# Kernel tuning notes

Measured on AMD Instinct MI355X. Metric: run time of the kernel, lower is better.

Reference implementation:

```python
import jax, jax.numpy as jnp
import numpy as np

B, S, D = 2, 2048, 3584
H, KV, HD = 28, 4, 128
N_REP = H // KV          # 7
MAX_S = 2048
SCALE = HD ** -0.5
ROPE_BASE = 1_000_000.0  # Qwen2 rope theta


def _rope_tables(max_s, hd, base):
    inv = 1.0 / (base ** (np.arange(0, hd, 2, dtype=np.float32) / hd))  # [hd/2]
    ang = np.arange(max_s, dtype=np.float32)[:, None] * inv[None, :]    # [S, hd/2]
    return jnp.asarray(np.cos(ang)), jnp.asarray(np.sin(ang))


def apply_rotary(x, cos, sin):
    # x: [b, s, h, hd] with interleaved complex pairs (torch view_as_complex layout)
    xr = x[..., 0::2]
    xi = x[..., 1::2]
    cos = cos[None, :, None, :]
    sin = sin[None, :, None, :]
    yr = xr * cos - xi * sin
    yi = xr * sin + xi * cos
    return jnp.stack([yr, yi], axis=-1).reshape(x.shape)


def setup_inputs() -> dict:
    key = jax.random.key(0)
    ks = jax.random.split(key, 8)
    w = 0.02
    x = jax.random.normal(ks[0], (B, S, D), jnp.float32)
    wq_w = jax.random.normal(ks[1], (H * HD, D), jnp.float32) * w
    wq_b = jax.random.normal(ks[2], (H * HD,), jnp.float32) * w
    wk_w = jax.random.normal(ks[3], (KV * HD, D), jnp.float32) * w
    wk_b = jax.random.normal(ks[4], (KV * HD,), jnp.float32) * w
    wv_w = jax.random.normal(ks[5], (KV * HD, D), jnp.float32) * w
    wv_b = jax.random.normal(ks[6], (KV * HD,), jnp.float32) * w
    wo_w = jax.random.normal(ks[7], (D, H * HD), jnp.float32) * w
    k_cache = jnp.zeros((B, MAX_S, KV, HD), jnp.float32)
    v_cache = jnp.zeros((B, MAX_S, KV, HD), jnp.float32)
    freqs_cos, freqs_sin = _rope_tables(MAX_S, HD, ROPE_BASE)
    # causal additive mask [s, t]; large-negative instead of -inf for safe grads
    mask = jnp.triu(jnp.full((S, S), -1e9, jnp.float32), k=1)
    return {"x": x, "wq_w": wq_w, "wq_b": wq_b, "wk_w": wk_w, "wk_b": wk_b,
            "wv_w": wv_w, "wv_b": wv_b, "wo_w": wo_w,
            "k_cache": k_cache, "v_cache": v_cache,
            "freqs_cos": freqs_cos, "freqs_sin": freqs_sin,
            "mask": mask, "start_pos": 0}


def reference(x, wq_w, wq_b, wk_w, wk_b, wv_w, wv_b, wo_w,
              k_cache, v_cache, freqs_cos, freqs_sin, mask, start_pos):
    bsz, seqlen, _ = x.shape
    end_pos = start_pos + seqlen
    q = (x @ wq_w.T + wq_b).reshape(bsz, seqlen, H, HD)
    k = (x @ wk_w.T + wk_b).reshape(bsz, seqlen, KV, HD)
    v = (x @ wv_w.T + wv_b).reshape(bsz, seqlen, KV, HD)
    cos = jax.lax.dynamic_slice_in_dim(freqs_cos, start_pos, seqlen, 0)
    sin = jax.lax.dynamic_slice_in_dim(freqs_sin, start_pos, seqlen, 0)
    q = apply_rotary(q, cos, sin)
    k = apply_rotary(k, cos, sin)
    # KV-cache write
    k_cache = jax.lax.dynamic_update_slice(k_cache, k, (0, start_pos, 0, 0))
    v_cache = jax.lax.dynamic_update_slice(v_cache, v, (0, start_pos, 0, 0))
    keys = k_cache[:bsz, :end_pos]    # [b, t, kv, hd]
    values = v_cache[:bsz, :end_pos]
    # GQA: repeat_interleave kv heads to n_heads
    keys = jnp.repeat(keys, N_REP, axis=2)      # [b, t, h, hd]
    values = jnp.repeat(values, N_REP, axis=2)
    scores = jnp.einsum('bshd,bthd->bsht', q, keys) * SCALE
    scores = scores + mask[None, :, None, :]
    probs = jax.nn.softmax(scores.astype(jnp.float32), axis=-1).astype(x.dtype)
    out = jnp.einsum('bsht,bthd->bshd', probs, values)
    out = out.reshape(bsz, seqlen, H * HD)
    return out @ wo_w.T
```

## Files before the change

### kernel.cpp

```cpp
#include <hip/hip_runtime.h>
#include <hip/hip_bf16.h>

typedef __attribute__((ext_vector_type(4)))  float  f32x4;
typedef __attribute__((ext_vector_type(16))) float  f32x16;
typedef __attribute__((ext_vector_type(8)))  __bf16 bf16x8;
typedef __attribute__((ext_vector_type(4)))  __bf16 bf16x4;
typedef __attribute__((ext_vector_type(4)))  unsigned int u32x4;

constexpr int S_LEN = 2048, DMODEL = 3584, NH = 28, NKV = 4, HD = 128, NREP = 7;
constexpr float SCALE_LOG2 = 0.1275174331f;

__device__ __forceinline__ unsigned int pack2(float a, float b) {
  unsigned short ua = __builtin_bit_cast(unsigned short, (__bf16)a);
  unsigned short ub = __builtin_bit_cast(unsigned short, (__bf16)b);
  return (unsigned int)ua | ((unsigned int)ub << 16);
}

__global__ void cvt5_kernel(const float* __restrict__ s0, const float* __restrict__ s1,
                            const float* __restrict__ s2, const float* __restrict__ s3,
                            const float* __restrict__ s4,
                            __bf16* __restrict__ d0, __bf16* __restrict__ d1,
                            __bf16* __restrict__ d2, __bf16* __restrict__ d3,
                            __bf16* __restrict__ d4,
                            int n0, int n1, int n2, int n3, int* __restrict__ ctr, int total) {
  if (blockIdx.x == 0 && threadIdx.x == 0) *ctr = 0;
  for (int i = blockIdx.x * blockDim.x + threadIdx.x; i < total; i += gridDim.x * blockDim.x) {
    const float* s; __bf16* d; int j = i;
    if (j < n0) { s = s0; d = d0; }
    else { j -= n0;
      if (j < n1) { s = s1; d = d1; }
      else { j -= n1;
        if (j < n2) { s = s2; d = d2; }
        else { j -= n2;
          if (j < n3) { s = s3; d = d3; }
          else { j -= n3; s = s4; d = d4; }
        }
      }
    }
    float4 v = reinterpret_cast<const float4*>(s)[j];
    bf16x4 o;
    o[0] = (__bf16)v.x; o[1] = (__bf16)v.y; o[2] = (__bf16)v.z; o[3] = (__bf16)v.w;
    reinterpret_cast<bf16x4*>(d)[j] = o;
  }
}

#define GLDS16(gsrc, ldst)                                                              \
  __builtin_amdgcn_global_load_lds((const __attribute__((address_space(1))) void*)(gsrc),\
                                   (__attribute__((address_space(3))) void*)(ldst), 16, 0, 0)

template <int MODE>
__global__ __launch_bounds__(512, 2) void gemm256(
    const __bf16* __restrict__ A, const __bf16* __restrict__ Bw,
    const float* __restrict__ bias, void* __restrict__ Cout,
    int M, int N, int K,
    const float* __restrict__ fcos, const float* __restrict__ fsin,
    const int* __restrict__ sp_ptr, float scale)
{
  extern __shared__ char smem[];
  const int tid = threadIdx.x;
  const int lane = tid & 63, wid = tid >> 6;
  const int wm = wid >> 2, wn = wid & 3;
  const int l31 = lane & 31, hh = lane >> 5;
  const int l15 = lane & 15;

  const int chunk = gridDim.x >> 3;
  const int wg = (blockIdx.x & 7) * chunk + (blockIdx.x >> 3);
  const int nbx = N >> 8;
  const int by = wg / nbx, bx = wg % nbx;
  const int row0 = by * 256, col0 = bx * 256;

  const int srL   = 16 * (tid >> 6) + ((tid >> 2) & 15);
  const int cperm = ((tid & 3) * 8) ^ (((tid >> 5) & 1) * 16);
  const __bf16* pA0 = A + (size_t)(row0 + srL) * K + cperm;
  const __bf16* pA1 = pA0 + (size_t)128 * K;
  const __bf16* pB0 = Bw + (size_t)(col0 + srL) * K + cperm;
  const __bf16* pB1 = pB0 + (size_t)128 * K;
  char* ldsA = smem + tid * 16;
  char* ldsB = smem + 65536 + tid * 16;

  const int laneoff = (l31 >> 4) * 1024 + l15 * 64 + hh * 16;
  const int ksx = (l31 & 8) << 2;
  const int abase = wm * 8192 + laneoff;
  const int R0 = wn * 64, R1 = wn * 64 + 32;
  const int bo0 = (R0 >> 7) * 8192 + ((R0 >> 4) & 7) * 1024;
  const int bo1 = (R1 >> 7) * 8192 + ((R1 >> 4) & 7) * 1024;

  f32x16 acc[4][2] = {};
  const int nt = K >> 5;

#pragma unroll
  for (int pt = 0; pt < 3; pt++) {
    const size_t ko = (size_t)pt * 32;
    char* sA = ldsA + pt * 16384;
    char* sB = ldsB + pt * 16384;
    GLDS16(pA0 + ko, sA);
    GLDS16(pA1 + ko, sA + 8192);
    GLDS16(pB0 + ko, sB);
    GLDS16(pB1 + ko, sB + 8192);
  }
  asm volatile("s_waitcnt vmcnt(8)" ::: "memory");
  __builtin_amdgcn_s_barrier();
  __builtin_amdgcn_sched_barrier(0);

  for (int t = 0; t < nt; t++) {
    const int slot = (t & 3) * 16384;
    const char* sa = smem + slot + abase;
    const char* sb = smem + slot + 65536 + laneoff;
    bf16x8 a0[4], a1[4], b0[2], b1[2];

    b0[0] = *reinterpret_cast<const bf16x8*>(sb + bo0 + ksx);
    b0[1] = *reinterpret_cast<const bf16x8*>(sb + bo1 + ksx);
#pragma unroll
    for (int fm = 0; fm < 4; fm++)
      a0[fm] = *reinterpret_cast<const bf16x8*>(sa + fm * 2048 + ksx);
    __builtin_amdgcn_sched_barrier(0);
    b1[0] = *reinterpret_cast<const bf16x8*>(sb + bo0 + (32 ^ ksx));
    b1[1] = *reinterpret_cast<const bf16x8*>(sb + bo1 + (32 ^ ksx));
#pragma unroll
    for (int fm = 0; fm < 4; fm++)
      a1[fm] = *reinterpret_cast<const bf16x8*>(sa + fm * 2048 + (32 ^ ksx));

    if (t + 3 < nt) {
      const size_t ko = (size_t)(t + 3) * 32;
      char* sA = ldsA + ((t + 3) & 3) * 16384;
      char* sB = ldsB + ((t + 3) & 3) * 16384;
      GLDS16(pA0 + ko, sA);
      GLDS16(pA1 + ko, sA + 8192);
      GLDS16(pB0 + ko, sB);
      GLDS16(pB1 + ko, sB + 8192);
    }

    asm volatile("s_waitcnt lgkmcnt(6)" ::: "memory");
    __builtin_amdgcn_sched_barrier(0);
    __builtin_amdgcn_s_setprio(1);
#pragma unroll
    for (int fn = 0; fn < 2; fn++)
#pragma unroll
      for (int fm = 0; fm < 4; fm++)
        acc[fm][fn] = __builtin_amdgcn_mfma_f32_32x32x16_bf16(a0[fm], b0[fn], acc[fm][fn], 0, 0, 0);
    __builtin_amdgcn_s_setprio(0);

    asm volatile("s_waitcnt lgkmcnt(0)" ::: "memory");
    __builtin_amdgcn_sched_barrier(0);
    __builtin_amdgcn_s_setprio(1);
#pragma unroll
    for (int fn = 0; fn < 2; fn++)
#pragma unroll
      for (int fm = 0; fm < 4; fm++)
        acc[fm][fn] = __builtin_amdgcn_mfma_f32_32x32x16_bf16(a1[fm], b1[fn], acc[fm][fn], 0, 0, 0);
    __builtin_amdgcn_s_setprio(0);

    if (t < nt - 3)       asm volatile("s_waitcnt vmcnt(8)" ::: "memory");
    else if (t == nt - 3) asm volatile("s_waitcnt vmcnt(4)" ::: "memory");
    else if (t == nt - 2) asm volatile("s_waitcnt vmcnt(0)" ::: "memory");
    __builtin_amdgcn_s_barrier();
    __builtin_amdgcn_sched_barrier(0);
  }

  if constexpr (MODE == 0) {
    float* C = (float*)Cout;
#pragma unroll
    for (int fm = 0; fm < 4; fm++) {
#pragma unroll
      for (int fn = 0; fn < 2; fn++) {
        const int col = col0 + wn * 64 + fn * 32 + l31;
#pragma unroll
        for (int r = 0; r < 16; r++) {
          const int row = row0 + wm * 128 + fm * 32 + (r & 3) + 8 * (r >> 2) + 4 * hh;
          C[(size_t)row * N + col] = acc[fm][fn][r];
        }
      }
    }
  } else {
    __bf16* C = (__bf16*)Cout;
    const int sp = sp_ptr[0];
    float bval[2];
#pragma unroll
    for (int fn = 0; fn < 2; fn++) bval[fn] = bias[col0 + wn * 64 + fn * 32 + l31];
#pragma unroll
    for (int fm = 0; fm < 4; fm++) {
#pragma unroll
      for (int fn = 0; fn < 2; fn++) {
        const int col = col0 + wn * 64 + fn * 32 + l31;
        const int i = (col & (HD - 1)) >> 1;
#pragma unroll
        for (int r = 0; r < 16; r++) {
          const int row = row0 + wm * 128 + fm * 32 + (r & 3) + 8 * (r >> 2) + 4 * hh;
          float y = acc[fm][fn][r] + bval[fn];
          float p = __shfl_xor(y, 1);
          const int spos = sp + (row & (S_LEN - 1));
          const float c = fcos[spos * (HD / 2) + i];
          const float sn = fsin[spos * (HD / 2) + i];
          y = (col & 1) ? (p * sn + y * c) : (y * c - p * sn);
          C[(size_t)row * N + col] = (__bf16)(y * scale);
        }
      }
    }
  }
}

__global__ __launch_bounds__(256) void gemm_kv(
    const __bf16* __restrict__ A,
    const __bf16* __restrict__ Wk, const float* __restrict__ bk, __bf16* __restrict__ Ko,
    const __bf16* __restrict__ Wv, const float* __restrict__ bv, __bf16* __restrict__ Vt,
    const float* __restrict__ fcos, const float* __restrict__ fsin,
    const int* __restrict__ sp_ptr)
{
  constexpr int N = 512, K = 3584;
  __shared__ __bf16 As[128 * 32];
  __shared__ __bf16 Bs[128 * 32];
  const int tid = threadIdx.x;
  const int lane = tid & 63, wid = tid >> 6;
  const int l15 = lane & 15, g = lane >> 4;
  const int wr = wid >> 1, wc = wid & 1;
  const bool isK = blockIdx.x < 4;
  const __bf16* Bw = isK ? Wk : Wv;
  const float* bias = isK ? bk : bv;
  const int row0 = blockIdx.y * 128;
  const int col0 = (blockIdx.x & 3) * 128;

  f32x4 acc[4][4] = {};

  const int srow = tid >> 2;
  const int scol = (tid & 3) * 8;
  const __bf16* Ag0 = A + (size_t)(row0 + srow) * K + scol;
  const __bf16* Ag1 = Ag0 + (size_t)64 * K;
  const __bf16* Bg0 = Bw + (size_t)(col0 + srow) * K + scol;
  const __bf16* Bg1 = Bg0 + (size_t)64 * K;
  __bf16* As0 = As + tid * 8;
  __bf16* As1 = As + 2048 + tid * 8;
  __bf16* Bs0 = Bs + tid * 8;
  __bf16* Bs1 = Bs + 2048 + tid * 8;

  for (int k0 = 0; k0 < K; k0 += 32) {
    GLDS16(Ag0 + k0, As0);
    GLDS16(Ag1 + k0, As1);
    GLDS16(Bg0 + k0, Bs0);
    GLDS16(Bg1 + k0, Bs1);
    __syncthreads();
    bf16x8 af[4], bfr[4];
#pragma unroll
    for (int m = 0; m < 4; m++)
      af[m] = *reinterpret_cast<const bf16x8*>(As + (wr * 64 + m * 16 + l15) * 32 + g * 8);
#pragma unroll
    for (int n = 0; n < 4; n++)
      bfr[n] = *reinterpret_cast<const bf16x8*>(Bs + (wc * 64 + n * 16 + l15) * 32 + g * 8);
#pragma unroll
    for (int m = 0; m < 4; m++)
#pragma unroll
      for (int n = 0; n < 4; n++)
        acc[m][n] = __builtin_amdgcn_mfma_f32_16x16x32_bf16(af[m], bfr[n], acc[m][n], 0, 0, 0);
    __syncthreads();
  }

  const int sp = sp_ptr[0];
  if (isK) {
#pragma unroll
    for (int m = 0; m < 4; m++) {
#pragma unroll
      for (int n = 0; n < 4; n++) {
        const int col = col0 + wc * 64 + n * 16 + l15;
        const float bval = bias[col];
        f32x4 v = acc[m][n];
#pragma unroll
        for (int r = 0; r < 4; r++) {
          const int row = row0 + wr * 64 + m * 16 + 4 * g + r;
          float y = v[r] + bval;
          float p = __shfl_xor(y, 1);
          const int i = (col & (HD - 1)) >> 1;
          const int spos = sp + (row & (S_LEN - 1));
          const float c = fcos[spos * (HD / 2) + i];
          const float sn = fsin[spos * (HD / 2) + i];
          y = (col & 1) ? (p * sn + y * c) : (y * c - p * sn);
          Ko[(size_t)row * N + col] = (__bf16)y;
        }
      }
    }
  } else {
    const int b4kv = ((row0 >> 11) * 4) + (blockIdx.x & 3);
    __bf16* vbase = Vt + ((size_t)b4kv << 18);
#pragma unroll
    for (int m = 0; m < 4; m++) {
#pragma unroll
      for (int n = 0; n < 4; n++) {
        const int d = wc * 64 + n * 16 + l15;
        const float bval = bias[col0 + d];
        const int s0 = (row0 + wr * 64 + m * 16 + 4 * g) & (S_LEN - 1);
        f32x4 v = acc[m][n];
        bf16x4 o;
#pragma unroll
        for (int r = 0; r < 4; r++) o[r] = (__bf16)(v[r] + bval);
        *reinterpret_cast<bf16x4*>(vbase + (size_t)d * S_LEN + s0) = o;
      }
    }
  }
}

__global__ __launch_bounds__(256, 2) void attn_kernel(
    const __bf16* __restrict__ Qb, const __bf16* __restrict__ Kb,
    const __bf16* __restrict__ Vt, __bf16* __restrict__ Ob, int* __restrict__ ctr)
{
  __shared__ __align__(16) char asmem[65536];
  __shared__ int jsh;

  const int tid = threadIdx.x, lane = tid & 63, wid = tid >> 6;
  const int l31 = lane & 31, hh = lane >> 5;

  const int trow = tid >> 4;
  const int kcol = (((tid & 15) * 16) ^ ((trow & 7) << 4)) >> 1;
  const int vrow = tid >> 3;
  const int vcol = (((tid & 7) * 16) ^ ((vrow & 7) << 4)) >> 1;

  constexpr int NITEMS = 16 * NH * 2;

  while (true) {
    if (tid == 0) jsh = atomicAdd(ctr, 1);
    __syncthreads();
    const int j = jsh;
    if (j >= NITEMS) break;

    const int qi = 15 - (j / 56);
    const int r56 = j % 56;
    const int h = r56 >> 1, b = r56 & 1;
    const int kvh = h / NREP;
    const int qw = qi * 128 + wid * 32;
    const int qg = qw + l31;

    const __bf16* Kbase = Kb + ((size_t)b * S_LEN * NKV + kvh) * HD;
    const __bf16* Vbase = Vt + ((size_t)b * NKV + kvh) * (size_t)HD * S_LEN;

    bf16x8 qf[8];
    {
      const __bf16* qp = Qb + (((size_t)b * S_LEN + qg) * NH + h) * HD + hh * 8;
#pragma unroll
      for (int c = 0; c < 8; c++) qf[c] = *reinterpret_cast<const bf16x8*>(qp + c * 16);
    }

    f32x16 o[4] = {};
    float mrun = -3.0e38f, lsum = 0.0f;

    const int ntiles = 2 * qi + 2;

#define STAGE(T, S)                                                                     \
    do {                                                                                \
      const int k0_ = (T) * 64;                                                         \
      char* Kd_ = asmem + (S) * 32768;                                                  \
      char* Vd_ = Kd_ + 16384;                                                          \
      _Pragma("unroll")                                                                 \
      for (int p = 0; p < 4; p++) {                                                     \
        GLDS16(Kbase + (size_t)(k0_ + p * 16 + trow) * (NKV * HD) + kcol,               \
               Kd_ + (p * 256 + tid) * 16);                                             \
        GLDS16(Vbase + (size_t)(p * 32 + vrow) * S_LEN + k0_ + vcol,                    \
               Vd_ + (p * 256 + tid) * 16);                                             \
      }                                                                                 \
    } while (0)

    STAGE(0, 0);

    for (int t = 0; t < ntiles; t++) {
      __syncthreads();
      if (t + 1 < ntiles) STAGE(t + 1, (t + 1) & 1);

      const char* Ksb = asmem + (t & 1) * 32768;
      const char* Vsb = Ksb + 16384;
      const int k0 = t * 64;

      f32x16 s0 = {}, s1 = {};
      {
        const char* kp0 = Ksb + l31 * 256;
        const char* kp1 = kp0 + 32 * 256;
        const int sw = (l31 & 7) << 4;
        __builtin_amdgcn_s_setprio(1);
#pragma unroll
        for (int c = 0; c < 8; c++) {
          const int cb = (c * 32 + hh * 16) ^ sw;
          bf16x8 kf0 = *reinterpret_cast<const bf16x8*>(kp0 + cb);
          s0 = __builtin_amdgcn_mfma_f32_32x32x16_bf16(kf0, qf[c], s0, 0, 0, 0);
          bf16x8 kf1 = *reinterpret_cast<const bf16x8*>(kp1 + cb);
          s1 = __builtin_amdgcn_mfma_f32_32x32x16_bf16(kf1, qf[c], s1, 0, 0, 0);
        }
        __builtin_amdgcn_s_setprio(0);
      }

      if (k0 + 63 > qw) {
#pragma unroll
        for (int r = 0; r < 16; r++) {
          const int kvo = k0 + ((r & 3) + 8 * (r >> 2)) + 4 * hh;
          if (kvo > qg)      s0[r] = -1.0e9f;
          if (kvo + 32 > qg) s1[r] = -1.0e9f;
        }
      }

      float pmax = -3.0e38f;
#pragma unroll
      for (int r = 0; r < 16; r++) { pmax = fmaxf(pmax, s0[r]); pmax = fmaxf(pmax, s1[r]); }
      pmax = fmaxf(pmax, __shfl_xor(pmax, 32));
      if (!__all(pmax <= mrun + 11.5f)) {
        const float mnew = fmaxf(mrun, pmax);
        const float fs = exp2f(mrun - mnew);
        lsum *= fs;
#pragma unroll
        for (int dt = 0; dt < 4; dt++) o[dt] *= fs;
        mrun = mnew;
      }
      float psum = 0.0f;
#pragma unroll
      for (int r = 0; r < 16; r++) {
        s0[r] = exp2f(s0[r] - mrun); psum += s0[r];
        s1[r] = exp2f(s1[r] - mrun); psum += s1[r];
      }
      lsum += psum;

      unsigned int pk[2][8], px[2][8];
#pragma unroll
      for (int jj = 0; jj < 8; jj++) {
        pk[0][jj] = pack2(s0[2 * jj], s0[2 * jj + 1]);
        pk[1][jj] = pack2(s1[2 * jj], s1[2 * jj + 1]);
      }
#pragma unroll
      for (int tt = 0; tt < 2; tt++)
#pragma unroll
        for (int jj = 0; jj < 8; jj++) px[tt][jj] = __shfl_xor(pk[tt][jj], 32);

      __builtin_amdgcn_s_setprio(1);
#pragma unroll
      for (int tt = 0; tt < 2; tt++) {
#pragma unroll
        for (int c2 = 0; c2 < 2; c2++) {
          u32x4 pb4;
          if (hh == 0)
            pb4 = (u32x4){pk[tt][4 * c2], pk[tt][4 * c2 + 1], px[tt][4 * c2], px[tt][4 * c2 + 1]};
          else
            pb4 = (u32x4){px[tt][4 * c2 + 2], px[tt][4 * c2 + 3], pk[tt][4 * c2 + 2], pk[tt][4 * c2 + 3]};
          bf16x8 pbf = __builtin_bit_cast(bf16x8, pb4);
          const int colb = tt * 64 + c2 * 32 + hh * 16;
#pragma unroll
          for (int dt = 0; dt < 4; dt++) {
            const int d = dt * 32 + l31;
            bf16x8 vf = *reinterpret_cast<const bf16x8*>(Vsb + d * 128 + (colb ^ ((d & 7) << 4)));
            o[dt] = __builtin_amdgcn_mfma_f32_32x32x16_bf16(vf, pbf, o[dt], 0, 0, 0);
          }
        }
      }
      __builtin_amdgcn_s_setprio(0);
    }
#undef STAGE

    lsum += __shfl_xor(lsum, 32);
    const float inv = 1.0f / lsum;
    char* my = asmem + wid * 8192;
#pragma unroll
    for (int dt = 0; dt < 4; dt++) {
#pragma unroll
      for (int jj = 0; jj < 8; jj++) {
        const int r = 2 * jj;
        const int d = dt * 32 + ((r & 3) + 8 * (r >> 2)) + 4 * hh;
        const unsigned int w = pack2(o[dt][r] * inv, o[dt][r + 1] * inv);
        *reinterpret_cast<unsigned int*>(my + ((l31 * 256 + d * 2) ^ ((l31 & 7) << 4))) = w;
      }
    }
#pragma unroll
    for (int jj = 0; jj < 8; jj++) {
      const int idx = jj * 64 + lane;
      const int row = idx >> 4, c16 = idx & 15;
      u32x4 val = *reinterpret_cast<u32x4*>(my + row * 256 + ((c16 * 16) ^ ((row & 7) << 4)));
      *reinterpret_cast<u32x4*>(Ob + (size_t)(b * S_LEN + qw + row) * (NH * HD) + h * HD + c16 * 8) = val;
    }
  }
}

extern "C" void kernel_launch(void* const* d_in, const int* in_sizes, int n_in,
                              void* d_out, int out_size, void* d_ws, size_t ws_size,
                              hipStream_t stream) {
  (void)in_sizes; (void)n_in; (void)out_size; (void)ws_size;
  const float* x    = (const float*)d_in[0];
  const float* wq_w = (const float*)d_in[1];
  const float* wq_b = (const float*)d_in[2];
  const float* wk_w = (const float*)d_in[3];
  const float* wk_b = (const float*)d_in[4];
  const float* wv_w = (const float*)d_in[5];
  const float* wv_b = (const float*)d_in[6];
  const float* wo_w = (const float*)d_in[7];
  const float* fcos = (const float*)d_in[10];
  const float* fsin = (const float*)d_in[11];
  const int*   spp  = (const int*)d_in[13];
  float* out = (float*)d_out;

  constexpr size_t XB_N = (size_t)4096 * 3584;
  constexpr size_t WQ_N = (size_t)3584 * 3584;
  constexpr size_t WK_N = (size_t)512 * 3584;
  constexpr size_t WO_N = (size_t)3584 * 3584;
  constexpr size_t KB_N = (size_t)4096 * 512;

  __bf16* xb  = (__bf16*)d_ws;
  __bf16* wqb = xb + XB_N;
  __bf16* wkb = wqb + WQ_N;
  __bf16* wvb = wkb + WK_N;
  __bf16* wob = wvb + WK_N;
  __bf16* Qb  = wob + WO_N;
  __bf16* Kb  = Qb + XB_N;
  __bf16* Vt  = Kb + KB_N;
  int*    ctr = (int*)(Vt + KB_N);
  __bf16* Ob  = xb;

  constexpr int N0 = (int)(XB_N / 4), N1 = (int)(WQ_N / 4), N2 = (int)(WK_N / 4),
                N3 = (int)(WK_N / 4), N4 = (int)(WO_N / 4);
  constexpr int NTOT = N0 + N1 + N2 + N3 + N4;
  cvt5_kernel<<<2048, 256, 0, stream>>>(x, wq_w, wk_w, wv_w, wo_w,
                                        xb, wqb, wkb, wvb, wob,
                                        N0, N1, N2, N3, ctr, NTOT);

  gemm256<2><<<dim3(224), 512, 131072, stream>>>(xb, wqb, wq_b, Qb, 4096, 3584, 3584,
                                                 fcos, fsin, spp, SCALE_LOG2);
  gemm_kv<<<dim3(8, 32), 256, 0, stream>>>(xb, wkb, wk_b, Kb, wvb, wv_b, Vt,
                                           fcos, fsin, spp);
  attn_kernel<<<dim3(512), 256, 0, stream>>>(Qb, Kb, Vt, Ob, ctr);
  gemm256<0><<<dim3(224), 512, 131072, stream>>>(Ob, wob, nullptr, out, 4096, 3584, 3584,
                                                 nullptr, nullptr, nullptr, 1.0f);
}
```

Before: 443.7 us.

## Shrink GEMM tile to 128x256 with 16x16 MFMA and triple-buffered LDS

```diff
diff --git a/kernel.cpp b/kernel.cpp
--- a/kernel.cpp
+++ b/kernel.cpp
@@ -49,7 +49,7 @@
                                    (__attribute__((address_space(3))) void*)(ldst), 16, 0, 0)
 
 template <int MODE>
-__global__ __launch_bounds__(512, 2) void gemm256(
+__global__ __launch_bounds__(512, 4) void gemm256(
     const __bf16* __restrict__ A, const __bf16* __restrict__ Bw,
     const float* __restrict__ bias, void* __restrict__ Cout,
     int M, int N, int K,
@@ -60,132 +60,125 @@
   const int tid = threadIdx.x;
   const int lane = tid & 63, wid = tid >> 6;
   const int wm = wid >> 2, wn = wid & 3;
-  const int l31 = lane & 31, hh = lane >> 5;
-  const int l15 = lane & 15;
+  const int l15 = lane & 15, g = (lane >> 4) & 3;
 
   const int chunk = gridDim.x >> 3;
   const int wg = (blockIdx.x & 7) * chunk + (blockIdx.x >> 3);
   const int nbx = N >> 8;
   const int by = wg / nbx, bx = wg % nbx;
-  const int row0 = by * 256, col0 = bx * 256;
+  const int row0 = by * 128, col0 = bx * 256;
 
   const int srL   = 16 * (tid >> 6) + ((tid >> 2) & 15);
   const int cperm = ((tid & 3) * 8) ^ (((tid >> 5) & 1) * 16);
-  const __bf16* pA0 = A + (size_t)(row0 + srL) * K + cperm;
-  const __bf16* pA1 = pA0 + (size_t)128 * K;
+  const __bf16* pA  = A + (size_t)(row0 + srL) * K + cperm;
   const __bf16* pB0 = Bw + (size_t)(col0 + srL) * K + cperm;
   const __bf16* pB1 = pB0 + (size_t)128 * K;
-  char* ldsA = smem + tid * 16;
-  char* ldsB = smem + 65536 + tid * 16;
-
-  const int laneoff = (l31 >> 4) * 1024 + l15 * 64 + hh * 16;
-  const int ksx = (l31 & 8) << 2;
-  const int abase = wm * 8192 + laneoff;
-  const int R0 = wn * 64, R1 = wn * 64 + 32;
-  const int bo0 = (R0 >> 7) * 8192 + ((R0 >> 4) & 7) * 1024;
-  const int bo1 = (R1 >> 7) * 8192 + ((R1 >> 4) & 7) * 1024;
-
-  f32x16 acc[4][2] = {};
+  char* ldsD = smem + tid * 16;
+
+  const int sw  = ((l15 >> 3) & 1) << 5;
+  const int rdo = l15 * 64 + ((g * 16) ^ sw);
+  const int aoff = wm * 4096 + rdo;
+  int bofs[4];
+#pragma unroll
+  for (int fn = 0; fn < 4; fn++) {
+    const int c = wn * 64 + fn * 16;
+    bofs[fn] = 8192 + (c >> 7) * 8192 + ((c >> 4) & 7) * 1024 + rdo;
+  }
+
+  f32x4 acc[4][4] = {};
   const int nt = K >> 5;
 
 #pragma unroll
-  for (int pt = 0; pt < 3; pt++) {
+  for (int pt = 0; pt < 2; pt++) {
     const size_t ko = (size_t)pt * 32;
-    char* sA = ldsA + pt * 16384;
-    char* sB = ldsB + pt * 16384;
-    GLDS16(pA0 + ko, sA);
-    GLDS16(pA1 + ko, sA + 8192);
-    GLDS16(pB0 + ko, sB);
-    GLDS16(pB1 + ko, sB + 8192);
-  }
-  asm volatile("s_waitcnt vmcnt(8)" ::: "memory");
+    char* base = ldsD + pt * 24576;
+    GLDS16(pA + ko, base);
+    GLDS16(pB0 + ko, base + 8192);
+    GLDS16(pB1 + ko, base + 16384);
+  }
+  asm volatile("s_waitcnt vmcnt(3)" ::: "memory");
   __builtin_amdgcn_s_barrier();
   __builtin_amdgcn_sched_barrier(0);
 
+  int sl = 0, sl2 = 2;
   for (int t = 0; t < nt; t++) {
-    const int slot = (t & 3) * 16384;
-    const char* sa = smem + slot + abase;
-    const char* sb = smem + slot + 65536 + laneoff;
-    bf16x8 a0[4], a1[4], b0[2], b1[2];
-
-    b0[0] = *reinterpret_cast<const bf16x8*>(sb + bo0 + ksx);
-    b0[1] = *reinterpret_cast<const bf16x8*>(sb + bo1 + ksx);
+    const char* sb = smem + sl * 24576;
+    bf16x8 af[4], bfv[4];
+
+    bfv[0] = *reinterpret_cast<const bf16x8*>(sb + bofs[0]);
+    bfv[1] = *reinterpret_cast<const bf16x8*>(sb + bofs[1]);
 #pragma unroll
     for (int fm = 0; fm < 4; fm++)
-      a0[fm] = *reinterpret_cast<const bf16x8*>(sa + fm * 2048 + ksx);
+      af[fm] = *reinterpret_cast<const bf16x8*>(sb + aoff + fm * 1024);
     __builtin_amdgcn_sched_barrier(0);
-    b1[0] = *reinterpret_cast<const bf16x8*>(sb + bo0 + (32 ^ ksx));
-    b1[1] = *reinterpret_cast<const bf16x8*>(sb + bo1 + (32 ^ ksx));
-#pragma unroll
-    for (int fm = 0; fm < 4; fm++)
-      a1[fm] = *reinterpret_cast<const bf16x8*>(sa + fm * 2048 + (32 ^ ksx));
-
-    if (t + 3 < nt) {
-      const size_t ko = (size_t)(t + 3) * 32;
-      char* sA = ldsA + ((t + 3) & 3) * 16384;
-      char* sB = ldsB + ((t + 3) & 3) * 16384;
-      GLDS16(pA0 + ko, sA);
-      GLDS16(pA1 + ko, sA + 8192);
-      GLDS16(pB0 + ko, sB);
-      GLDS16(pB1 + ko, sB + 8192);
-    }
-
-    asm volatile("s_waitcnt lgkmcnt(6)" ::: "memory");
+    bfv[2] = *reinterpret_cast<const bf16x8*>(sb + bofs[2]);
+    bfv[3] = *reinterpret_cast<const bf16x8*>(sb + bofs[3]);
+
+    if (t + 2 < nt) {
+      const size_t ko = (size_t)(t + 2) * 32;
+      char* base = ldsD + sl2 * 24576;
+      GLDS16(pA + ko, base);
+      GLDS16(pB0 + ko, base + 8192);
+      GLDS16(pB1 + ko, base + 16384);
+    }
+
+    asm volatile("s_waitcnt lgkmcnt(2)" ::: "memory");
     __builtin_amdgcn_sched_barrier(0);
     __builtin_amdgcn_s_setprio(1);
 #pragma unroll
     for (int fn = 0; fn < 2; fn++)
 #pragma unroll
       for (int fm = 0; fm < 4; fm++)
-        acc[fm][fn] = __builtin_amdgcn_mfma_f32_32x32x16_bf16(a0[fm], b0[fn], acc[fm][fn], 0, 0, 0);
+        acc[fm][fn] = __builtin_amdgcn_mfma_f32_16x16x32_bf16(af[fm], bfv[fn], acc[fm][fn], 0, 0, 0);
     __builtin_amdgcn_s_setprio(0);
 
     asm volatile("s_waitcnt lgkmcnt(0)" ::: "memory");
     __builtin_amdgcn_sched_barrier(0);
     __builtin_amdgcn_s_setprio(1);
 #pragma unroll
-    for (int fn = 0; fn < 2; fn++)
+    for (int fn = 2; fn < 4; fn++)
 #pragma unroll
       for (int fm = 0; fm < 4; fm++)
-        acc[fm][fn] = __builtin_amdgcn_mfma_f32_32x32x16_bf16(a1[fm], b1[fn], acc[fm][fn], 0, 0, 0);
+        acc[fm][fn] = __builtin_amdgcn_mfma_f32_16x16x32_bf16(af[fm], bfv[fn], acc[fm][fn], 0, 0, 0);
     __builtin_amdgcn_s_setprio(0);
 
-    if (t < nt - 3)       asm volatile("s_waitcnt vmcnt(8)" ::: "memory");
-    else if (t == nt - 3) asm volatile("s_waitcnt vmcnt(4)" ::: "memory");
+    if (t < nt - 2)       asm volatile("s_waitcnt vmcnt(3)" ::: "memory");
     else if (t == nt - 2) asm volatile("s_waitcnt vmcnt(0)" ::: "memory");
     __builtin_amdgcn_s_barrier();
     __builtin_amdgcn_sched_barrier(0);
+
+    sl = (sl == 2) ? 0 : sl + 1;
+    sl2 = (sl2 == 2) ? 0 : sl2 + 1;
   }
 
   if constexpr (MODE == 0) {
     float* C = (float*)Cout;
 #pragma unroll
     for (int fm = 0; fm < 4; fm++) {
-#pragma unroll
-      for (int fn = 0; fn < 2; fn++) {
-        const int col = col0 + wn * 64 + fn * 32 + l31;
-#pragma unroll
-        for (int r = 0; r < 16; r++) {
-          const int row = row0 + wm * 128 + fm * 32 + (r & 3) + 8 * (r >> 2) + 4 * hh;
-          C[(size_t)row * N + col] = acc[fm][fn][r];
-        }
+      const int row = row0 + wm * 64 + fm * 16 + 4 * g;
+#pragma unroll
+      for (int fn = 0; fn < 4; fn++) {
+        const int col = col0 + wn * 64 + fn * 16 + l15;
+#pragma unroll
+        for (int r = 0; r < 4; r++)
+          C[(size_t)(row + r) * N + col] = acc[fm][fn][r];
       }
     }
   } else {
     __bf16* C = (__bf16*)Cout;
     const int sp = sp_ptr[0];
-    float bval[2];
-#pragma unroll
-    for (int fn = 0; fn < 2; fn++) bval[fn] = bias[col0 + wn * 64 + fn * 32 + l31];
+    float bval[4];
+#pragma unroll
+    for (int fn = 0; fn < 4; fn++) bval[fn] = bias[col0 + wn * 64 + fn * 16 + l15];
 #pragma unroll
     for (int fm = 0; fm < 4; fm++) {
 #pragma unroll
-      for (int fn = 0; fn < 2; fn++) {
-        const int col = col0 + wn * 64 + fn * 32 + l31;
+      for (int fn = 0; fn < 4; fn++) {
+        const int col = col0 + wn * 64 + fn * 16 + l15;
         const int i = (col & (HD - 1)) >> 1;
 #pragma unroll
-        for (int r = 0; r < 16; r++) {
-          const int row = row0 + wm * 128 + fm * 32 + (r & 3) + 8 * (r >> 2) + 4 * hh;
+        for (int r = 0; r < 4; r++) {
+          const int row = row0 + wm * 64 + fm * 16 + 4 * g + r;
           float y = acc[fm][fn][r] + bval[fn];
           float p = __shfl_xor(y, 1);
           const int spos = sp + (row & (S_LEN - 1));
@@ -510,11 +503,11 @@
                                         xb, wqb, wkb, wvb, wob,
                                         N0, N1, N2, N3, ctr, NTOT);
 
-  gemm256<2><<<dim3(224), 512, 131072, stream>>>(xb, wqb, wq_b, Qb, 4096, 3584, 3584,
-                                                 fcos, fsin, spp, SCALE_LOG2);
+  gemm256<2><<<dim3(448), 512, 73728, stream>>>(xb, wqb, wq_b, Qb, 4096, 3584, 3584,
+                                                fcos, fsin, spp, SCALE_LOG2);
   gemm_kv<<<dim3(8, 32), 256, 0, stream>>>(xb, wkb, wk_b, Kb, wvb, wv_b, Vt,
                                            fcos, fsin, spp);
   attn_kernel<<<dim3(512), 256, 0, stream>>>(Qb, Kb, Vt, Ob, ctr);
-  gemm256<0><<<dim3(224), 512, 131072, stream>>>(Ob, wob, nullptr, out, 4096, 3584, 3584,
-                                                 nullptr, nullptr, nullptr, 1.0f);
+  gemm256<0><<<dim3(448), 512, 73728, stream>>>(Ob, wob, nullptr, out, 4096, 3584, 3584,
+                                                nullptr, nullptr, nullptr, 1.0f);
 }
```

Result: slower. 455.4 us (+2.6%).
